# Kernel optimization log

Hardware: AMD Instinct MI355X
Metric: run time of the kernel (lower is better)

Reference implementation:

```python
import jax, jax.numpy as jnp
import numpy as np

N = 4096      # num nodes/docs (<= max_compare=5000, so no random subsampling)
IN = 768      # input feature dim
OUT = 512     # projector output dim
TEM = 0.5     # temperature
BN_EPS = 1e-5
NORM_EPS = 1e-12


def setup_inputs() -> dict:
    key = jax.random.key(0)
    ks = jax.random.split(key, 5)
    doc0 = jax.random.normal(ks[0], (N, IN), dtype=jnp.float32)
    doc1 = jax.random.normal(ks[1], (N, IN), dtype=jnp.float32)
    doc2 = jax.random.normal(ks[2], (N, IN), dtype=jnp.float32)
    # 6 freshly-initialized projectors (one per view per pair, as in the torch forward)
    W1s = jax.random.normal(ks[3], (6, IN, OUT), dtype=jnp.float32) * 0.05
    b1s = jnp.zeros((6, OUT), dtype=jnp.float32)
    gammas = jnp.ones((6, OUT), dtype=jnp.float32)
    betas = jnp.zeros((6, OUT), dtype=jnp.float32)
    W2s = jax.random.normal(ks[4], (6, OUT, OUT), dtype=jnp.float32) * 0.05
    b2s = jnp.zeros((6, OUT), dtype=jnp.float32)
    return {"doc0": doc0, "doc1": doc1, "doc2": doc2,
            "W1s": W1s, "b1s": b1s, "gammas": gammas, "betas": betas,
            "W2s": W2s, "b2s": b2s}


def _projector(x, W1, b1, g, b, W2, b2):
    # Linear -> BatchNorm1d (training-mode batch stats) -> ReLU -> Linear
    h = x @ W1 + b1
    mu = h.mean(axis=0)
    var = h.var(axis=0)  # biased, matching torch BN normalization
    h = (h - mu) * jax.lax.rsqrt(var + BN_EPS) * g + b
    h = jax.nn.relu(h)
    return h @ W2 + b2


def _l2norm(x):
    n = jnp.sqrt(jnp.sum(x * x, axis=1, keepdims=True))
    return x / jnp.maximum(n, NORM_EPS)


def _pair_loss(a, b):
    # a, b: [N, OUT], already L2-normalized.
    # Full-matrix form of the chunked batch_loss (mathematically identical).
    refl = jnp.exp((a @ a.T) / TEM)      # [N, N]
    between = jnp.exp((a @ b.T) / TEM)   # [N, N]
    pos = jnp.diagonal(between)
    denom = refl.sum(axis=1) + between.sum(axis=1) - jnp.diagonal(refl)
    return -jnp.log(pos / denom)


def reference(doc0, doc1, doc2, W1s, b1s, gammas, betas, W2s, b2s):
    docs = [doc0, doc1, doc2]
    pairs = [(0, 1), (0, 2), (1, 2)]
    total = jnp.float32(0.0)
    k = 0
    for (i, j) in pairs:
        o1 = _l2norm(_projector(docs[i], W1s[k], b1s[k], gammas[k], betas[k], W2s[k], b2s[k]))
        k += 1
        o2 = _l2norm(_projector(docs[j], W1s[k], b1s[k], gammas[k], betas[k], W2s[k], b2s[k]))
        k += 1
        l = 0.5 * (_pair_loss(o1, o2) + _pair_loss(o2, o1))
        total = total + l.mean()
    return total / 3.0
```

## Files before the change

kernel.cpp:

```cpp
#include <hip/hip_runtime.h>
#include <hip/hip_bf16.h>
#include <hip/hip_fp8.h>

#define N_ROWS 4096
#define IN_DIM 768
#define OUT_DIM 512


using bf16x8 = __attribute__((ext_vector_type(8))) short;
using f32x4  = __attribute__((ext_vector_type(4))) float;
using i64    = long;
using i64x2  = __attribute__((ext_vector_type(2))) long;

__device__ __constant__ int c_docmap[6] = {0, 1, 0, 2, 1, 2};

__device__ inline unsigned short f2bf(float f) {
    __hip_bfloat16 h = __float2bfloat16(f);
    return reinterpret_cast<unsigned short&>(h);
}
__device__ inline float bf2f(unsigned short u) {
    return __uint_as_float((unsigned int)u << 16);
}
__device__ inline unsigned char f2fp8(float f) {
    __hip_fp8_e4m3 t(f);
    return t.__x;
}
__device__ inline uint4 pack8bf(const float* v) {
    uint4 o;
    unsigned short* p = (unsigned short*)&o;
#pragma unroll
    for (int j = 0; j < 8; ++j) p[j] = f2bf(v[j]);
    return o;
}

__global__ __launch_bounds__(256) void prep(
    const float* __restrict__ d0, const float* __restrict__ d1,
    const float* __restrict__ d2, const float* __restrict__ W1s,
    const float* __restrict__ W2s, unsigned short* __restrict__ Xb,
    unsigned short* __restrict__ W1t, unsigned short* __restrict__ W2t,
    char* __restrict__ zbase) {
    int wunit = blockIdx.x * 4 + (threadIdx.x >> 6);
    int lane = threadIdx.x & 63;
    int lane15 = lane & 15, quad = lane >> 4;
    if (wunit < 18432) {
        int d = wunit / 6144, u = wunit % 6144;
        int gt = u / 24, kf = u % 24;
        const float* src = (d == 0) ? d0 : ((d == 1) ? d1 : d2);
        const float* s = src + (size_t)(gt * 16 + lane15) * IN_DIM + kf * 32 + quad * 8;
        float4 a = *(const float4*)s, b = *(const float4*)(s + 4);
        float v[8] = {a.x, a.y, a.z, a.w, b.x, b.y, b.z, b.w};
        *(uint4*)(Xb + (size_t)d * N_ROWS * IN_DIM + (size_t)u * 512 + lane * 8) = pack8bf(v);
    } else if (wunit < 23040) {
        int v0 = wunit - 18432;
        int z = v0 / 768, u = v0 % 768;
        int gt = u / 24, kf = u % 24;
        int n = gt * 16 + lane15;
        int k0 = kf * 32 + quad * 8;
        const float* W = W1s + (size_t)z * IN_DIM * OUT_DIM;
        float v[8];
#pragma unroll
        for (int j = 0; j < 8; ++j) v[j] = W[(size_t)(k0 + j) * OUT_DIM + n];
        *(uint4*)(W1t + (size_t)z * OUT_DIM * IN_DIM + (size_t)u * 512 + lane * 8) = pack8bf(v);
    } else if (wunit < 26112) {
        int v0 = wunit - 23040;
        int z = v0 / 512, u = v0 % 512;
        int gt = u / 16, kf = u % 16;
        int n = gt * 16 + lane15;
        int k0 = kf * 32 + quad * 8;
        const float* W = W2s + (size_t)z * OUT_DIM * OUT_DIM;
        float v[8];
#pragma unroll
        for (int j = 0; j < 8; ++j) v[j] = W[(size_t)(k0 + j) * OUT_DIM + n];
        *(uint4*)(W2t + (size_t)z * OUT_DIM * OUT_DIM + (size_t)u * 512 + lane * 8) = pack8bf(v);
    } else {
        size_t b = (size_t)(wunit - 26112) * 1024 + (size_t)lane * 16;
        if (b < (size_t)(24576 + 98304))
            *(float4*)(zbase + b) = (float4){0.f, 0.f, 0.f, 0.f};
    }
}

__global__ __launch_bounds__(256) void gemm1_bn(
    const unsigned short* __restrict__ Xb, const unsigned short* __restrict__ W1t,
    const float* __restrict__ biasAll, unsigned short* __restrict__ H,
    float* __restrict__ stats) {
    const int NKF = IN_DIM / 32;
    int px = blockIdx.x;
    int logical = (px & 7) * 96 + (px >> 3);
    int T = logical >> 1, sub = logical & 1;
    int z = T >> 6, rem = T & 63;
    int m0 = (rem >> 2) * 256, n0 = (rem & 3) * 128;
    const unsigned short* A = Xb + (size_t)c_docmap[z] * N_ROWS * IN_DIM;
    const unsigned short* B = W1t + (size_t)z * OUT_DIM * IN_DIM;
    const float* bz = biasAll + (size_t)z * OUT_DIM;
    unsigned short* C = H + (size_t)z * N_ROWS * OUT_DIM;

    int tid = threadIdx.x;
    int wave = (tid >> 6) + sub * 4, lane = tid & 63;
    int lane15 = lane & 15, quad = lane >> 4;
    int wrow = (wave >> 1) * 64, wcol = (wave & 1) * 64;

    const unsigned short* Ca = A + (size_t)((m0 + wrow) >> 4) * NKF * 512 + (size_t)lane * 8;
    const unsigned short* Cb = B + (size_t)((n0 + wcol) >> 4) * NKF * 512 + (size_t)lane * 8;

    f32x4 acc[4][4];
#pragma unroll
    for (int mt = 0; mt < 4; ++mt)
#pragma unroll
        for (int nt = 0; nt < 4; ++nt)
            acc[mt][nt] = (f32x4){0.f, 0.f, 0.f, 0.f};

    bf16x8 aC[4], bC[4], aN[4], bN[4];
#pragma unroll
    for (int t = 0; t < 4; ++t) {
        aC[t] = *(const bf16x8*)(Ca + (size_t)t * NKF * 512);
        bC[t] = *(const bf16x8*)(Cb + (size_t)t * NKF * 512);
    }
#pragma unroll
    for (int kf = 0; kf < NKF; ++kf) {
        if (kf < NKF - 1) {
#pragma unroll
            for (int t = 0; t < 4; ++t) {
                aN[t] = *(const bf16x8*)(Ca + (size_t)t * NKF * 512 + (kf + 1) * 512);
                bN[t] = *(const bf16x8*)(Cb + (size_t)t * NKF * 512 + (kf + 1) * 512);
            }
        }
        __builtin_amdgcn_s_setprio(1);
#pragma unroll
        for (int mt = 0; mt < 4; ++mt)
#pragma unroll
            for (int nt = 0; nt < 4; ++nt)
                acc[mt][nt] = __builtin_amdgcn_mfma_f32_16x16x32_bf16(aC[mt], bC[nt], acc[mt][nt], 0, 0, 0);
        __builtin_amdgcn_s_setprio(0);
#pragma unroll
        for (int t = 0; t < 4; ++t) { aC[t] = aN[t]; bC[t] = bN[t]; }
    }

    float s1[4] = {0.f, 0.f, 0.f, 0.f}, s2[4] = {0.f, 0.f, 0.f, 0.f};
#pragma unroll
    for (int nt = 0; nt < 4; ++nt) {
        int col = n0 + wcol + nt * 16 + lane15;
        float bv = bz[col];
#pragma unroll
        for (int mt = 0; mt < 4; ++mt)
#pragma unroll
            for (int r = 0; r < 4; ++r) {
                int row = m0 + wrow + mt * 16 + quad * 4 + r;
                float v = acc[mt][nt][r] + bv;
                C[(size_t)row * OUT_DIM + col] = f2bf(v);
                s1[nt] += v; s2[nt] += v * v;
            }
    }
#pragma unroll
    for (int nt = 0; nt < 4; ++nt) {
        float a = s1[nt], b = s2[nt];
        a += __shfl_xor(a, 16); a += __shfl_xor(a, 32);
        b += __shfl_xor(b, 16); b += __shfl_xor(b, 32);
        if (quad == 0) {
            int col = n0 + wcol + nt * 16 + lane15;
            atomicAdd(&stats[((size_t)z * OUT_DIM + col) * 2 + 0], a);
            atomicAdd(&stats[((size_t)z * OUT_DIM + col) * 2 + 1], b);
        }
    }
}

__global__ __launch_bounds__(256) void bn_apply(
    const unsigned short* __restrict__ H, unsigned short* __restrict__ Hb,
    const float* __restrict__ stats, const float* __restrict__ gammas,
    const float* __restrict__ betas) {
    int wunit = blockIdx.x * 4 + (threadIdx.x >> 6);
    if (wunit >= 24576) return;
    int lane = threadIdx.x & 63;
    int lane15 = lane & 15, quad = lane >> 4;
    int z = wunit / 4096, u = wunit % 4096;
    int gt = u / 16, kf = u % 16;
    int row = gt * 16 + lane15;
    int k = kf * 32 + quad * 8;
    uint4 hu = *(const uint4*)(H + ((size_t)z * N_ROWS + row) * OUT_DIM + k);
    unsigned int w[4] = {hu.x, hu.y, hu.z, hu.w};
    float v[8];
#pragma unroll
    for (int j = 0; j < 8; ++j) {
        unsigned short us = (j & 1) ? (unsigned short)(w[j >> 1] >> 16)
                                    : (unsigned short)(w[j >> 1] & 0xffff);
        size_t sc = (size_t)z * OUT_DIM + k + j;
        float mu = stats[sc * 2 + 0] * (1.f / N_ROWS);
        float var = stats[sc * 2 + 1] * (1.f / N_ROWS) - mu * mu;
        float s = gammas[sc] * rsqrtf(var + 1e-5f);
        v[j] = fmaxf(fmaf(bf2f(us), s, betas[sc] - mu * s), 0.f);
    }
    *(uint4*)(Hb + (size_t)z * N_ROWS * OUT_DIM + (size_t)u * 512 + lane * 8) = pack8bf(v);
}

__global__ __launch_bounds__(512) void gemm2_fused(
    const unsigned short* __restrict__ Hb, const unsigned short* __restrict__ W2t,
    const float* __restrict__ biasAll, unsigned char* __restrict__ Abuf) {
    const int NKF = OUT_DIM / 32;
    int px = blockIdx.x;
    int L = (px & 7) * 48 + (px >> 3);
    int z = L >> 6;
    int m0 = (L & 63) * 64;
    const unsigned short* A = Hb + (size_t)z * N_ROWS * OUT_DIM;
    const unsigned short* B = W2t + (size_t)z * OUT_DIM * OUT_DIM;
    const float* bz = biasAll + (size_t)z * OUT_DIM;
    unsigned char* Az = Abuf + (size_t)z * N_ROWS * OUT_DIM;

    int tid = threadIdx.x;
    int wave = tid >> 6, lane = tid & 63;
    int lane15 = lane & 15, quad = lane >> 4;
    int wcol = wave * 64;

    const unsigned short* Ca = A + (size_t)(m0 >> 4) * NKF * 512 + (size_t)lane * 8;
    const unsigned short* Cb = B + (size_t)(wave * 4) * NKF * 512 + (size_t)lane * 8;

    f32x4 acc[4][4];
#pragma unroll
    for (int mt = 0; mt < 4; ++mt)
#pragma unroll
        for (int nt = 0; nt < 4; ++nt)
            acc[mt][nt] = (f32x4){0.f, 0.f, 0.f, 0.f};

    bf16x8 aC[4], bC[4], aN[4], bN[4];
#pragma unroll
    for (int t = 0; t < 4; ++t) {
        aC[t] = *(const bf16x8*)(Ca + (size_t)t * NKF * 512);
        bC[t] = *(const bf16x8*)(Cb + (size_t)t * NKF * 512);
    }
#pragma unroll
    for (int kf = 0; kf < NKF; ++kf) {
        if (kf < NKF - 1) {
#pragma unroll
            for (int t = 0; t < 4; ++t) {
                aN[t] = *(const bf16x8*)(Ca + (size_t)t * NKF * 512 + (kf + 1) * 512);
                bN[t] = *(const bf16x8*)(Cb + (size_t)t * NKF * 512 + (kf + 1) * 512);
            }
        }
#pragma unroll
        for (int mt = 0; mt < 4; ++mt)
#pragma unroll
            for (int nt = 0; nt < 4; ++nt)
                acc[mt][nt] = __builtin_amdgcn_mfma_f32_16x16x32_bf16(aC[mt], bC[nt], acc[mt][nt], 0, 0, 0);
#pragma unroll
        for (int t = 0; t < 4; ++t) { aC[t] = aN[t]; bC[t] = bN[t]; }
    }

    __shared__ float part[8][64];
    __shared__ float scf[64];
    __shared__ __attribute__((aligned(16))) unsigned char T[64 * 520];

    float rs[16];
#pragma unroll
    for (int j = 0; j < 16; ++j) rs[j] = 0.f;
#pragma unroll
    for (int nt = 0; nt < 4; ++nt) {
        float bv = bz[wcol + nt * 16 + lane15];
#pragma unroll
        for (int mt = 0; mt < 4; ++mt)
#pragma unroll
            for (int r = 0; r < 4; ++r) {
                float v = acc[mt][nt][r] + bv;
                acc[mt][nt][r] = v;
                rs[mt * 4 + r] += v * v;
            }
    }
#pragma unroll
    for (int j = 0; j < 16; ++j) {
        float v = rs[j];
        v += __shfl_xor(v, 1); v += __shfl_xor(v, 2);
        v += __shfl_xor(v, 4); v += __shfl_xor(v, 8);
        rs[j] = v;
    }
    if (lane15 == 0) {
#pragma unroll
        for (int j = 0; j < 16; ++j)
            part[wave][(j >> 2) * 16 + quad * 4 + (j & 3)] = rs[j];
    }
    __syncthreads();
    if (tid < 64) {
        float ss = 0.f;
#pragma unroll
        for (int w = 0; w < 8; ++w) ss += part[w][tid];
        scf[tid] = 1.f / fmaxf(sqrtf(ss), 1e-12f);
    }
    __syncthreads();
#pragma unroll
    for (int mt = 0; mt < 4; ++mt)
#pragma unroll
        for (int r = 0; r < 4; ++r) {
            int row = mt * 16 + quad * 4 + r;
            float s = scf[row];
#pragma unroll
            for (int nt = 0; nt < 4; ++nt)
                T[row * 520 + wcol + nt * 16 + lane15] = f2fp8(acc[mt][nt][r] * s);
        }
    __syncthreads();
#pragma unroll
    for (int gt = 0; gt < 4; ++gt) {
        int row = gt * 16 + lane15;
        i64 lo = *(const i64*)(T + row * 520 + (2 * wave) * 32 + quad * 8);
        i64 hi = *(const i64*)(T + row * 520 + (2 * wave + 1) * 32 + quad * 8);
        i64x2 st; st[0] = lo; st[1] = hi;
        int gtg = (m0 >> 4) + gt;
        *(i64x2*)(Az + ((size_t)(gtg * 8 + wave) * 64 + lane) * 16) = st;
    }
}

__global__ __launch_bounds__(256) void gram_kernel(const unsigned char* __restrict__ Abase,
                                                   float* __restrict__ rowsum,
                                                   float* __restrict__ crossdot) {
    int px = blockIdx.x;
    int logical = (px & 7) * 792 + (px >> 3);
    int tile = logical >> 1, sub = logical & 1;
    int p = tile / 1056;
    int t0 = tile - p * 1056;
    const unsigned char* Cm = Abase + (size_t)p * 2 * N_ROWS * OUT_DIM;

    int I = 0;
    while (t0 >= 64 - 2 * I) { t0 -= 64 - 2 * I; ++I; }
    int J = 2 * I + t0;
    int m0 = I * 256, n0 = J * 128;

    int tid = threadIdx.x;
    int wave = (tid >> 6) + sub * 4, lane = tid & 63;
    int lane15 = lane & 15, quad = lane >> 4;
    int wrow = (wave >> 1) * 64, wcol = (wave & 1) * 64;

    const unsigned char* Ca = Cm + (size_t)((m0 + wrow) >> 4) * 8192 + (size_t)lane * 16;
    const unsigned char* Cb = Cm + (size_t)((n0 + wcol) >> 4) * 8192 + (size_t)lane * 16;

    f32x4 acc[4][4];
#pragma unroll
    for (int mt = 0; mt < 4; ++mt)
#pragma unroll
        for (int nt = 0; nt < 4; ++nt)
            acc[mt][nt] = (f32x4){0.f, 0.f, 0.f, 0.f};

    i64x2 aC[4], bC[4], aN[4], bN[4];
#pragma unroll
    for (int t = 0; t < 4; ++t) {
        aC[t] = *(const i64x2*)(Ca + (size_t)t * 8192);
        bC[t] = *(const i64x2*)(Cb + (size_t)t * 8192);
    }
#pragma unroll
    for (int kh = 0; kh < 8; ++kh) {
        if (kh < 7) {
#pragma unroll
            for (int t = 0; t < 4; ++t) {
                aN[t] = *(const i64x2*)(Ca + (size_t)t * 8192 + (kh + 1) * 1024);
                bN[t] = *(const i64x2*)(Cb + (size_t)t * 8192 + (kh + 1) * 1024);
            }
        }
        __builtin_amdgcn_s_setprio(1);
#pragma unroll
        for (int half = 0; half < 2; ++half)
#pragma unroll
            for (int mt = 0; mt < 4; ++mt)
#pragma unroll
                for (int nt = 0; nt < 4; ++nt)
                    acc[mt][nt] = __builtin_amdgcn_mfma_f32_16x16x32_fp8_fp8(
                        aC[mt][half], bC[nt][half], acc[mt][nt], 0, 0, 0);
        __builtin_amdgcn_s_setprio(0);
#pragma unroll
        for (int t = 0; t < 4; ++t) { aC[t] = aN[t]; bC[t] = bN[t]; }
    }

    float* cdp = crossdot + (size_t)p * 2 * N_ROWS;
    float* rp  = rowsum  + (size_t)p * 2 * N_ROWS;

    float rs[16];
    float cs[4] = {0.f, 0.f, 0.f, 0.f};
#pragma unroll
    for (int j = 0; j < 16; ++j) rs[j] = 0.f;

    if (J >= 2 * I + 2) {
#pragma unroll
        for (int mt = 0; mt < 4; ++mt)
#pragma unroll
            for (int nt = 0; nt < 4; ++nt)
#pragma unroll
                for (int r = 0; r < 4; ++r) {
                    float e = __expf(2.f * acc[mt][nt][r]);
                    rs[mt * 4 + r] += e;
                    cs[nt] += e;
                }
        if (J >= 32 && ((J - 32) >> 1) == I) {
#pragma unroll
            for (int mt = 0; mt < 4; ++mt)
#pragma unroll
                for (int nt = 0; nt < 4; ++nt) {
                    int gcol = n0 + wcol + nt * 16 + lane15;
#pragma unroll
                    for (int r = 0; r < 4; ++r) {
                        int grow = m0 + wrow + mt * 16 + quad * 4 + r;
                        if (gcol == grow + N_ROWS) {
                            float s = acc[mt][nt][r];
                            cdp[grow] = s;
                            cdp[gcol] = s;
                        }
                    }
                }
        }
    } else {
#pragma unroll
        for (int mt = 0; mt < 4; ++mt)
#pragma unroll
            for (int nt = 0; nt < 4; ++nt) {
                int gcol = n0 + wcol + nt * 16 + lane15;
#pragma unroll
                for (int r = 0; r < 4; ++r) {
                    int grow = m0 + wrow + mt * 16 + quad * 4 + r;
                    if (grow < gcol) {
                        float e = __expf(2.f * acc[mt][nt][r]);
                        rs[mt * 4 + r] += e;
                        cs[nt] += e;
                    }
                }
            }
    }

#pragma unroll
    for (int j = 0; j < 16; ++j) {
        float v = rs[j];
        v += __shfl_xor(v, 1); v += __shfl_xor(v, 2);
        v += __shfl_xor(v, 4); v += __shfl_xor(v, 8);
        rs[j] = v;
    }
    if (lane15 == 0) {
#pragma unroll
        for (int j = 0; j < 16; ++j) {
            int grow = m0 + wrow + (j >> 2) * 16 + quad * 4 + (j & 3);
            atomicAdd(&rp[grow], rs[j]);
        }
    }
#pragma unroll
    for (int n = 0; n < 4; ++n) {
        float v = cs[n];
        v += __shfl_xor(v, 16); v += __shfl_xor(v, 32);
        cs[n] = v;
    }
    if (quad == 0) {
#pragma unroll
        for (int n = 0; n < 4; ++n) {
            int gcol = n0 + wcol + n * 16 + lane15;
            atomicAdd(&rp[gcol], cs[n]);
        }
    }
}

__global__ void loss_kernel(const float* __restrict__ rowsum,
                            const float* __restrict__ crossdot, float* __restrict__ out) {
    int i = blockIdx.x * 256 + threadIdx.x;
    float v = logf(rowsum[i]) - 2.f * crossdot[i];
#pragma unroll
    for (int m = 1; m < 64; m <<= 1) v += __shfl_xor(v, m);
    __shared__ float red[4];
    if ((threadIdx.x & 63) == 0) red[threadIdx.x >> 6] = v;
    __syncthreads();
    if (threadIdx.x == 0)
        atomicAdd(out, (red[0] + red[1] + red[2] + red[3]) * (1.f / 24576.f));
}

extern "C" void kernel_launch(void* const* d_in, const int* in_sizes, int n_in,
                              void* d_out, int out_size, void* d_ws, size_t ws_size,
                              hipStream_t stream) {
    const float* doc0   = (const float*)d_in[0];
    const float* doc1   = (const float*)d_in[1];
    const float* doc2   = (const float*)d_in[2];
    const float* W1s    = (const float*)d_in[3];
    const float* b1s    = (const float*)d_in[4];
    const float* gammas = (const float*)d_in[5];
    const float* betas  = (const float*)d_in[6];
    const float* W2s    = (const float*)d_in[7];
    const float* b2s    = (const float*)d_in[8];
    float* out = (float*)d_out;

    char* base = (char*)d_ws;
    size_t off = 0;
    auto alloc = [&](size_t bytes) -> char* {
        char* r = base + off;
        off += (bytes + 255) & ~(size_t)255;
        return r;
    };

    unsigned short* Xb   = (unsigned short*)alloc((size_t)3 * N_ROWS * IN_DIM * 2);
    unsigned short* W1t  = (unsigned short*)alloc((size_t)6 * OUT_DIM * IN_DIM * 2);
    unsigned short* W2t  = (unsigned short*)alloc((size_t)6 * OUT_DIM * OUT_DIM * 2);
    unsigned short* H    = (unsigned short*)alloc((size_t)6 * N_ROWS * OUT_DIM * 2);
    unsigned short* Hb   = (unsigned short*)alloc((size_t)6 * N_ROWS * OUT_DIM * 2);
    unsigned char*  Abuf = (unsigned char*)Xb;
    char* zbase = alloc(24576 + 98304);
    float* stats  = (float*)zbase;
    float* rowsum = (float*)(zbase + 24576);
    float* cdot   = (float*)alloc((size_t)3 * 2 * N_ROWS * 4);

    if (ws_size < off) return;

    hipMemsetAsync(out, 0, sizeof(float), stream);

    prep<<<6558, 256, 0, stream>>>(doc0, doc1, doc2, W1s, W2s, Xb, W1t, W2t, zbase);

    gemm1_bn<<<768, 256, 0, stream>>>(Xb, W1t, b1s, H, stats);

    bn_apply<<<6144, 256, 0, stream>>>(H, Hb, stats, gammas, betas);

    gemm2_fused<<<384, 512, 0, stream>>>(Hb, W2t, b2s, Abuf);

    gram_kernel<<<6336, 256, 0, stream>>>(Abuf, rowsum, cdot);

    loss_kernel<<<96, 256, 0, stream>>>(rowsum, cdot, out);
}
```

Measured before the change: 281.7 us.

## Drop register double-buffering, raise occupancy, and make fp8 A layout k-major

Replaces the explicit register prefetch (current/next fragment double-buffering and setprio) in gemm1, gemm2 and the gram kernel with simple non-unrolled loops that load fragments each iteration, and adds a minimum of 3 blocks per CU to the launch bounds of gemm1 and the gram kernel. The aim is to cut register pressure so more waves stay resident and latency is hidden by occupancy rather than software pipelining. It also reorders the fp8 normalized-embedding buffer so each k-slice is contiguous across all row groups, and changes the gram kernel's addressing to match. The risk is exposed load latency inside each wave now that loads no longer overlap the MFMAs.

```diff
diff --git a/kernel.cpp b/kernel.cpp
--- a/kernel.cpp
+++ b/kernel.cpp
@@ -79,7 +79,7 @@
     }
 }
 
-__global__ __launch_bounds__(256) void gemm1_bn(
+__global__ __launch_bounds__(256, 3) void gemm1_bn(
     const unsigned short* __restrict__ Xb, const unsigned short* __restrict__ W1t,
     const float* __restrict__ biasAll, unsigned short* __restrict__ H,
     float* __restrict__ stats) {
@@ -109,30 +109,19 @@
         for (int nt = 0; nt < 4; ++nt)
             acc[mt][nt] = (f32x4){0.f, 0.f, 0.f, 0.f};
 
-    bf16x8 aC[4], bC[4], aN[4], bN[4];
-#pragma unroll
-    for (int t = 0; t < 4; ++t) {
-        aC[t] = *(const bf16x8*)(Ca + (size_t)t * NKF * 512);
-        bC[t] = *(const bf16x8*)(Cb + (size_t)t * NKF * 512);
-    }
-#pragma unroll
+#pragma unroll 1
     for (int kf = 0; kf < NKF; ++kf) {
-        if (kf < NKF - 1) {
-#pragma unroll
-            for (int t = 0; t < 4; ++t) {
-                aN[t] = *(const bf16x8*)(Ca + (size_t)t * NKF * 512 + (kf + 1) * 512);
-                bN[t] = *(const bf16x8*)(Cb + (size_t)t * NKF * 512 + (kf + 1) * 512);
-            }
-        }
-        __builtin_amdgcn_s_setprio(1);
+        bf16x8 a[4], b[4];
+#pragma unroll
+        for (int t = 0; t < 4; ++t) {
+            a[t] = *(const bf16x8*)(Ca + (size_t)t * NKF * 512 + (size_t)kf * 512);
+            b[t] = *(const bf16x8*)(Cb + (size_t)t * NKF * 512 + (size_t)kf * 512);
+        }
 #pragma unroll
         for (int mt = 0; mt < 4; ++mt)
 #pragma unroll
             for (int nt = 0; nt < 4; ++nt)
-                acc[mt][nt] = __builtin_amdgcn_mfma_f32_16x16x32_bf16(aC[mt], bC[nt], acc[mt][nt], 0, 0, 0);
-        __builtin_amdgcn_s_setprio(0);
-#pragma unroll
-        for (int t = 0; t < 4; ++t) { aC[t] = aN[t]; bC[t] = bN[t]; }
+                acc[mt][nt] = __builtin_amdgcn_mfma_f32_16x16x32_bf16(a[mt], b[nt], acc[mt][nt], 0, 0, 0);
     }
 
     float s1[4] = {0.f, 0.f, 0.f, 0.f}, s2[4] = {0.f, 0.f, 0.f, 0.f};
@@ -219,28 +208,19 @@
         for (int nt = 0; nt < 4; ++nt)
             acc[mt][nt] = (f32x4){0.f, 0.f, 0.f, 0.f};
 
-    bf16x8 aC[4], bC[4], aN[4], bN[4];
-#pragma unroll
-    for (int t = 0; t < 4; ++t) {
-        aC[t] = *(const bf16x8*)(Ca + (size_t)t * NKF * 512);
-        bC[t] = *(const bf16x8*)(Cb + (size_t)t * NKF * 512);
-    }
-#pragma unroll
+#pragma unroll 1
     for (int kf = 0; kf < NKF; ++kf) {
-        if (kf < NKF - 1) {
-#pragma unroll
-            for (int t = 0; t < 4; ++t) {
-                aN[t] = *(const bf16x8*)(Ca + (size_t)t * NKF * 512 + (kf + 1) * 512);
-                bN[t] = *(const bf16x8*)(Cb + (size_t)t * NKF * 512 + (kf + 1) * 512);
-            }
+        bf16x8 a[4], b[4];
+#pragma unroll
+        for (int t = 0; t < 4; ++t) {
+            a[t] = *(const bf16x8*)(Ca + (size_t)t * NKF * 512 + (size_t)kf * 512);
+            b[t] = *(const bf16x8*)(Cb + (size_t)t * NKF * 512 + (size_t)kf * 512);
         }
 #pragma unroll
         for (int mt = 0; mt < 4; ++mt)
 #pragma unroll
             for (int nt = 0; nt < 4; ++nt)
-                acc[mt][nt] = __builtin_amdgcn_mfma_f32_16x16x32_bf16(aC[mt], bC[nt], acc[mt][nt], 0, 0, 0);
-#pragma unroll
-        for (int t = 0; t < 4; ++t) { aC[t] = aN[t]; bC[t] = bN[t]; }
+                acc[mt][nt] = __builtin_amdgcn_mfma_f32_16x16x32_bf16(a[mt], b[nt], acc[mt][nt], 0, 0, 0);
     }
 
     __shared__ float part[8][64];
@@ -300,13 +280,13 @@
         i64 hi = *(const i64*)(T + row * 520 + (2 * wave + 1) * 32 + quad * 8);
         i64x2 st; st[0] = lo; st[1] = hi;
         int gtg = (m0 >> 4) + gt;
-        *(i64x2*)(Az + ((size_t)(gtg * 8 + wave) * 64 + lane) * 16) = st;
-    }
-}
-
-__global__ __launch_bounds__(256) void gram_kernel(const unsigned char* __restrict__ Abase,
-                                                   float* __restrict__ rowsum,
-                                                   float* __restrict__ crossdot) {
+        *(i64x2*)(Az + ((size_t)(wave * 256 + gtg) * 64 + lane) * 16) = st;
+    }
+}
+
+__global__ __launch_bounds__(256, 3) void gram_kernel(const unsigned char* __restrict__ Abase,
+                                                      float* __restrict__ rowsum,
+                                                      float* __restrict__ crossdot) {
     int px = blockIdx.x;
     int logical = (px & 7) * 792 + (px >> 3);
     int tile = logical >> 1, sub = logical & 1;
@@ -324,8 +304,11 @@
     int lane15 = lane & 15, quad = lane >> 4;
     int wrow = (wave >> 1) * 64, wcol = (wave & 1) * 64;
 
-    const unsigned char* Ca = Cm + (size_t)((m0 + wrow) >> 4) * 8192 + (size_t)lane * 16;
-    const unsigned char* Cb = Cm + (size_t)((n0 + wcol) >> 4) * 8192 + (size_t)lane * 16;
+    int gA = (m0 + wrow) >> 4, gB = (n0 + wcol) >> 4;
+    const unsigned char* Ca = Cm + (size_t)(gA >> 8) * N_ROWS * OUT_DIM
+                                 + (size_t)(gA & 255) * 1024 + (size_t)lane * 16;
+    const unsigned char* Cb = Cm + (size_t)(gB >> 8) * N_ROWS * OUT_DIM
+                                 + (size_t)(gB & 255) * 1024 + (size_t)lane * 16;
 
     f32x4 acc[4][4];
 #pragma unroll
@@ -334,22 +317,14 @@
         for (int nt = 0; nt < 4; ++nt)
             acc[mt][nt] = (f32x4){0.f, 0.f, 0.f, 0.f};
 
-    i64x2 aC[4], bC[4], aN[4], bN[4];
-#pragma unroll
-    for (int t = 0; t < 4; ++t) {
-        aC[t] = *(const i64x2*)(Ca + (size_t)t * 8192);
-        bC[t] = *(const i64x2*)(Cb + (size_t)t * 8192);
-    }
-#pragma unroll
+#pragma unroll 1
     for (int kh = 0; kh < 8; ++kh) {
-        if (kh < 7) {
-#pragma unroll
-            for (int t = 0; t < 4; ++t) {
-                aN[t] = *(const i64x2*)(Ca + (size_t)t * 8192 + (kh + 1) * 1024);
-                bN[t] = *(const i64x2*)(Cb + (size_t)t * 8192 + (kh + 1) * 1024);
-            }
-        }
-        __builtin_amdgcn_s_setprio(1);
+        i64x2 a[4], b[4];
+#pragma unroll
+        for (int t = 0; t < 4; ++t) {
+            a[t] = *(const i64x2*)(Ca + (size_t)kh * 262144 + t * 1024);
+            b[t] = *(const i64x2*)(Cb + (size_t)kh * 262144 + t * 1024);
+        }
 #pragma unroll
         for (int half = 0; half < 2; ++half)
 #pragma unroll
@@ -357,10 +332,7 @@
 #pragma unroll
                 for (int nt = 0; nt < 4; ++nt)
                     acc[mt][nt] = __builtin_amdgcn_mfma_f32_16x16x32_fp8_fp8(
-                        aC[mt][half], bC[nt][half], acc[mt][nt], 0, 0, 0);
-        __builtin_amdgcn_s_setprio(0);
-#pragma unroll
-        for (int t = 0; t < 4; ++t) { aC[t] = aN[t]; bC[t] = bN[t]; }
+                        a[mt][half], b[nt][half], acc[mt][nt], 0, 0, 0);
     }
 
     float* cdp = crossdot + (size_t)p * 2 * N_ROWS;
```

After: 297.5 us. +5.6%, slower.

## Enlarge gram tile per wave to 128x64 and relayout fp8 buffer k-major

Applied to the files above, without the earlier changes.

Each gram block now computes a full 256x128 tile with four waves, each owning 128x64 (8x4 MFMA tiles) instead of splitting the tile across two blocks. The fp8 normalized-embedding buffer written by gemm2 is reordered so k-groups are outermost, letting each wave stream contiguous row-group chunks per k step. Grid size halves, launch_bounds requests 2 blocks per CU, setprio is dropped and the k-loop is no longer unrolled. The intent is higher operand reuse and fewer loads per MFMA, paid for with much higher register pressure (128 accumulator floats plus 24 operand vectors) and possibly lower occupancy or spills.

```diff
diff --git a/kernel.cpp b/kernel.cpp
--- a/kernel.cpp
+++ b/kernel.cpp
@@ -300,18 +300,17 @@
         i64 hi = *(const i64*)(T + row * 520 + (2 * wave + 1) * 32 + quad * 8);
         i64x2 st; st[0] = lo; st[1] = hi;
         int gtg = (m0 >> 4) + gt;
-        *(i64x2*)(Az + ((size_t)(gtg * 8 + wave) * 64 + lane) * 16) = st;
-    }
-}
-
-__global__ __launch_bounds__(256) void gram_kernel(const unsigned char* __restrict__ Abase,
-                                                   float* __restrict__ rowsum,
-                                                   float* __restrict__ crossdot) {
+        *(i64x2*)(Az + ((size_t)(wave * 256 + gtg) * 64 + lane) * 16) = st;
+    }
+}
+
+__global__ __launch_bounds__(256, 2) void gram_kernel(const unsigned char* __restrict__ Abase,
+                                                      float* __restrict__ rowsum,
+                                                      float* __restrict__ crossdot) {
     int px = blockIdx.x;
-    int logical = (px & 7) * 792 + (px >> 3);
-    int tile = logical >> 1, sub = logical & 1;
-    int p = tile / 1056;
-    int t0 = tile - p * 1056;
+    int logical = (px & 7) * 396 + (px >> 3);
+    int p = logical / 1056;
+    int t0 = logical - p * 1056;
     const unsigned char* Cm = Abase + (size_t)p * 2 * N_ROWS * OUT_DIM;
 
     int I = 0;
@@ -320,60 +319,65 @@
     int m0 = I * 256, n0 = J * 128;
 
     int tid = threadIdx.x;
-    int wave = (tid >> 6) + sub * 4, lane = tid & 63;
+    int wave = tid >> 6, lane = tid & 63;
     int lane15 = lane & 15, quad = lane >> 4;
-    int wrow = (wave >> 1) * 64, wcol = (wave & 1) * 64;
-
-    const unsigned char* Ca = Cm + (size_t)((m0 + wrow) >> 4) * 8192 + (size_t)lane * 16;
-    const unsigned char* Cb = Cm + (size_t)((n0 + wcol) >> 4) * 8192 + (size_t)lane * 16;
-
-    f32x4 acc[4][4];
-#pragma unroll
-    for (int mt = 0; mt < 4; ++mt)
+    int R0 = m0 + (wave >> 1) * 128;
+    int C0 = n0 + (wave & 1) * 64;
+
+    int gA = R0 >> 4, gB = C0 >> 4;
+    const unsigned char* Ca = Cm + (size_t)(gA >> 8) * N_ROWS * OUT_DIM
+                                 + (size_t)(gA & 255) * 1024 + (size_t)lane * 16;
+    const unsigned char* Cb = Cm + (size_t)(gB >> 8) * N_ROWS * OUT_DIM
+                                 + (size_t)(gB & 255) * 1024 + (size_t)lane * 16;
+
+    f32x4 acc[8][4];
+#pragma unroll
+    for (int mt = 0; mt < 8; ++mt)
 #pragma unroll
         for (int nt = 0; nt < 4; ++nt)
             acc[mt][nt] = (f32x4){0.f, 0.f, 0.f, 0.f};
 
-    i64x2 aC[4], bC[4], aN[4], bN[4];
-#pragma unroll
-    for (int t = 0; t < 4; ++t) {
-        aC[t] = *(const i64x2*)(Ca + (size_t)t * 8192);
-        bC[t] = *(const i64x2*)(Cb + (size_t)t * 8192);
-    }
-#pragma unroll
+    i64x2 aC[8], bC[4], aN[8], bN[4];
+#pragma unroll
+    for (int t = 0; t < 8; ++t) aC[t] = *(const i64x2*)(Ca + (size_t)t * 1024);
+#pragma unroll
+    for (int t = 0; t < 4; ++t) bC[t] = *(const i64x2*)(Cb + (size_t)t * 1024);
+
+#pragma unroll 1
     for (int kh = 0; kh < 8; ++kh) {
         if (kh < 7) {
 #pragma unroll
-            for (int t = 0; t < 4; ++t) {
-                aN[t] = *(const i64x2*)(Ca + (size_t)t * 8192 + (kh + 1) * 1024);
-                bN[t] = *(const i64x2*)(Cb + (size_t)t * 8192 + (kh + 1) * 1024);
-            }
-        }
-        __builtin_amdgcn_s_setprio(1);
+            for (int t = 0; t < 8; ++t)
+                aN[t] = *(const i64x2*)(Ca + (size_t)(kh + 1) * 262144 + t * 1024);
+#pragma unroll
+            for (int t = 0; t < 4; ++t)
+                bN[t] = *(const i64x2*)(Cb + (size_t)(kh + 1) * 262144 + t * 1024);
+        }
 #pragma unroll
         for (int half = 0; half < 2; ++half)
 #pragma unroll
-            for (int mt = 0; mt < 4; ++mt)
+            for (int mt = 0; mt < 8; ++mt)
 #pragma unroll
                 for (int nt = 0; nt < 4; ++nt)
                     acc[mt][nt] = __builtin_amdgcn_mfma_f32_16x16x32_fp8_fp8(
                         aC[mt][half], bC[nt][half], acc[mt][nt], 0, 0, 0);
-        __builtin_amdgcn_s_setprio(0);
-#pragma unroll
-        for (int t = 0; t < 4; ++t) { aC[t] = aN[t]; bC[t] = bN[t]; }
+#pragma unroll
+        for (int t = 0; t < 8; ++t) aC[t] = aN[t];
+#pragma unroll
+        for (int t = 0; t < 4; ++t) bC[t] = bN[t];
     }
 
     float* cdp = crossdot + (size_t)p * 2 * N_ROWS;
     float* rp  = rowsum  + (size_t)p * 2 * N_ROWS;
 
-    float rs[16];
+    float rs[32];
     float cs[4] = {0.f, 0.f, 0.f, 0.f};
 #pragma unroll
-    for (int j = 0; j < 16; ++j) rs[j] = 0.f;
+    for (int j = 0; j < 32; ++j) rs[j] = 0.f;
 
     if (J >= 2 * I + 2) {
 #pragma unroll
-        for (int mt = 0; mt < 4; ++mt)
+        for (int mt = 0; mt < 8; ++mt)
 #pragma unroll
             for (int nt = 0; nt < 4; ++nt)
 #pragma unroll
@@ -384,13 +388,13 @@
                 }
         if (J >= 32 && ((J - 32) >> 1) == I) {
 #pragma unroll
-            for (int mt = 0; mt < 4; ++mt)
+            for (int mt = 0; mt < 8; ++mt)
 #pragma unroll
                 for (int nt = 0; nt < 4; ++nt) {
-                    int gcol = n0 + wcol + nt * 16 + lane15;
+                    int gcol = C0 + nt * 16 + lane15;
 #pragma unroll
                     for (int r = 0; r < 4; ++r) {
-                        int grow = m0 + wrow + mt * 16 + quad * 4 + r;
+                        int grow = R0 + mt * 16 + quad * 4 + r;
                         if (gcol == grow + N_ROWS) {
                             float s = acc[mt][nt][r];
                             cdp[grow] = s;
@@ -401,13 +405,13 @@
         }
     } else {
 #pragma unroll
-        for (int mt = 0; mt < 4; ++mt)
+        for (int mt = 0; mt < 8; ++mt)
 #pragma unroll
             for (int nt = 0; nt < 4; ++nt) {
-                int gcol = n0 + wcol + nt * 16 + lane15;
+                int gcol = C0 + nt * 16 + lane15;
 #pragma unroll
                 for (int r = 0; r < 4; ++r) {
-                    int grow = m0 + wrow + mt * 16 + quad * 4 + r;
+                    int grow = R0 + mt * 16 + quad * 4 + r;
                     if (grow < gcol) {
                         float e = __expf(2.f * acc[mt][nt][r]);
                         rs[mt * 4 + r] += e;
@@ -418,7 +422,7 @@
     }
 
 #pragma unroll
-    for (int j = 0; j < 16; ++j) {
+    for (int j = 0; j < 32; ++j) {
         float v = rs[j];
         v += __shfl_xor(v, 1); v += __shfl_xor(v, 2);
         v += __shfl_xor(v, 4); v += __shfl_xor(v, 8);
@@ -426,8 +430,8 @@
     }
     if (lane15 == 0) {
 #pragma unroll
-        for (int j = 0; j < 16; ++j) {
-            int grow = m0 + wrow + (j >> 2) * 16 + quad * 4 + (j & 3);
+        for (int j = 0; j < 32; ++j) {
+            int grow = R0 + (j >> 2) * 16 + quad * 4 + (j & 3);
             atomicAdd(&rp[grow], rs[j]);
         }
     }
@@ -440,7 +444,7 @@
     if (quad == 0) {
 #pragma unroll
         for (int n = 0; n < 4; ++n) {
-            int gcol = n0 + wcol + n * 16 + lane15;
+            int gcol = C0 + n * 16 + lane15;
             atomicAdd(&rp[gcol], cs[n]);
         }
     }
@@ -504,7 +508,7 @@
 
     gemm2_fused<<<384, 512, 0, stream>>>(Hb, W2t, b2s, Abuf);
 
-    gram_kernel<<<6336, 256, 0, stream>>>(Abuf, rowsum, cdot);
+    gram_kernel<<<3168, 256, 0, stream>>>(Abuf, rowsum, cdot);
 
     loss_kernel<<<96, 256, 0, stream>>>(rowsum, cdot, out);
 }
```

Measured after the change: 315.4 us. +11.9%, slower.

## Reorder fp8 operand layout k-major and stagger k-chunks per wave in gram kernel

Applied to the files above, without the earlier changes.

Changes the packed fp8 operand layout so each k-chunk (wave index) holds all row-groups contiguously, and updates the gram kernel addressing to match. The gram loop becomes a non-unrolled loop without explicit prefetch double-buffering. Each wave starts at a different k-chunk to spread memory accesses across channels. Adds a launch-bounds occupancy hint of 3 blocks per CU. The aim is to cut register pressure and raise occupancy, at the cost of losing software prefetch and the priority hints.

```diff
diff --git a/kernel.cpp b/kernel.cpp
--- a/kernel.cpp
+++ b/kernel.cpp
@@ -300,13 +300,13 @@
         i64 hi = *(const i64*)(T + row * 520 + (2 * wave + 1) * 32 + quad * 8);
         i64x2 st; st[0] = lo; st[1] = hi;
         int gtg = (m0 >> 4) + gt;
-        *(i64x2*)(Az + ((size_t)(gtg * 8 + wave) * 64 + lane) * 16) = st;
-    }
-}
-
-__global__ __launch_bounds__(256) void gram_kernel(const unsigned char* __restrict__ Abase,
-                                                   float* __restrict__ rowsum,
-                                                   float* __restrict__ crossdot) {
+        *(i64x2*)(Az + ((size_t)(wave * 256 + gtg) * 64 + lane) * 16) = st;
+    }
+}
+
+__global__ __launch_bounds__(256, 3) void gram_kernel(const unsigned char* __restrict__ Abase,
+                                                      float* __restrict__ rowsum,
+                                                      float* __restrict__ crossdot) {
     int px = blockIdx.x;
     int logical = (px & 7) * 792 + (px >> 3);
     int tile = logical >> 1, sub = logical & 1;
@@ -324,8 +324,11 @@
     int lane15 = lane & 15, quad = lane >> 4;
     int wrow = (wave >> 1) * 64, wcol = (wave & 1) * 64;
 
-    const unsigned char* Ca = Cm + (size_t)((m0 + wrow) >> 4) * 8192 + (size_t)lane * 16;
-    const unsigned char* Cb = Cm + (size_t)((n0 + wcol) >> 4) * 8192 + (size_t)lane * 16;
+    int gA = (m0 + wrow) >> 4, gB = (n0 + wcol) >> 4;
+    const unsigned char* Ca = Cm + (size_t)(gA >> 8) * N_ROWS * OUT_DIM
+                                 + (size_t)(gA & 255) * 1024 + (size_t)lane * 16;
+    const unsigned char* Cb = Cm + (size_t)(gB >> 8) * N_ROWS * OUT_DIM
+                                 + (size_t)(gB & 255) * 1024 + (size_t)lane * 16;
 
     f32x4 acc[4][4];
 #pragma unroll
@@ -334,22 +337,17 @@
         for (int nt = 0; nt < 4; ++nt)
             acc[mt][nt] = (f32x4){0.f, 0.f, 0.f, 0.f};
 
-    i64x2 aC[4], bC[4], aN[4], bN[4];
-#pragma unroll
-    for (int t = 0; t < 4; ++t) {
-        aC[t] = *(const i64x2*)(Ca + (size_t)t * 8192);
-        bC[t] = *(const i64x2*)(Cb + (size_t)t * 8192);
-    }
-#pragma unroll
-    for (int kh = 0; kh < 8; ++kh) {
-        if (kh < 7) {
-#pragma unroll
-            for (int t = 0; t < 4; ++t) {
-                aN[t] = *(const i64x2*)(Ca + (size_t)t * 8192 + (kh + 1) * 1024);
-                bN[t] = *(const i64x2*)(Cb + (size_t)t * 8192 + (kh + 1) * 1024);
-            }
-        }
-        __builtin_amdgcn_s_setprio(1);
+    int khoff = wave;
+#pragma unroll 1
+    for (int t = 0; t < 8; ++t) {
+        int kh = (t + khoff) & 7;
+        int kbase = kh << 18;
+        i64x2 a[4], b[4];
+#pragma unroll
+        for (int u = 0; u < 4; ++u) {
+            a[u] = *(const i64x2*)(Ca + kbase + u * 1024);
+            b[u] = *(const i64x2*)(Cb + kbase + u * 1024);
+        }
 #pragma unroll
         for (int half = 0; half < 2; ++half)
 #pragma unroll
@@ -357,10 +355,7 @@
 #pragma unroll
                 for (int nt = 0; nt < 4; ++nt)
                     acc[mt][nt] = __builtin_amdgcn_mfma_f32_16x16x32_fp8_fp8(
-                        aC[mt][half], bC[nt][half], acc[mt][nt], 0, 0, 0);
-        __builtin_amdgcn_s_setprio(0);
-#pragma unroll
-        for (int t = 0; t < 4; ++t) { aC[t] = aN[t]; bC[t] = bN[t]; }
+                        a[mt][half], b[nt][half], acc[mt][nt], 0, 0, 0);
     }
 
     float* cdp = crossdot + (size_t)p * 2 * N_ROWS;
```

Result: slower. 297.6 us (+5.7%).
